# Kernel optimization log

Measured on AMD Instinct MI355X. Metric: run time of the kernel, lower is better.

The kernel has to match this reference:

```python
import jax, jax.numpy as jnp
import numpy as np

V, E, HD, T = 50000, 300, 512, 9   # vocab, embed_dim, hidden_dim, tagset
H = HD // 2                         # per-direction LSTM hidden
B, S = 64, 512


def _uniform(key, shape, k):
    return jax.random.uniform(key, shape, jnp.float32, -k, k)


def setup_inputs() -> dict:
    key = jax.random.key(0)
    ks = jax.random.split(key, 16)
    klstm = 1.0 / np.sqrt(H)
    kout = 1.0 / np.sqrt(HD)
    embed = jax.random.normal(ks[0], (V, E), jnp.float32) * 0.1
    embed = embed.at[0].set(0.0)  # padding_idx=0
    inp = {
        'sentence': jax.random.randint(ks[1], (B, S), 1, V),
        'tags': jax.random.randint(ks[2], (B, S), 0, T),
        'embed': embed,
        'wih_f': _uniform(ks[3], (4 * H, E), klstm),
        'whh_f': _uniform(ks[4], (4 * H, H), klstm),
        'bih_f': _uniform(ks[5], (4 * H,), klstm),
        'bhh_f': _uniform(ks[6], (4 * H,), klstm),
        'wih_b': _uniform(ks[7], (4 * H, E), klstm),
        'whh_b': _uniform(ks[8], (4 * H, H), klstm),
        'bih_b': _uniform(ks[9], (4 * H,), klstm),
        'bhh_b': _uniform(ks[10], (4 * H,), klstm),
        'w_out': _uniform(ks[11], (T, HD), kout),
        'b_out': _uniform(ks[12], (T,), kout),
        'start_trans': _uniform(ks[13], (T,), 0.1),
        'end_trans': _uniform(ks[14], (T,), 0.1),
        'trans': _uniform(ks[15], (T, T), 0.1),
    }
    # contiguous left-aligned mask with random lengths (mask[:,0]==1 as torchcrf requires)
    lengths = jax.random.randint(jax.random.fold_in(key, 99), (B,), S // 2, S + 1)
    inp['mask'] = (jnp.arange(S)[None, :] < lengths[:, None]).astype(jnp.int32)
    return inp


def _lstm(x, wih, whh, bih, bhh):
    # x: [S,B,E] -> hidden states [S,B,H]; gate order i,f,g,o (PyTorch)
    b = x.shape[1]
    def step(carry, xt):
        h, c = carry
        g = xt @ wih.T + h @ whh.T + (bih + bhh)
        i, f, gg, o = jnp.split(g, 4, axis=-1)
        c = jax.nn.sigmoid(f) * c + jax.nn.sigmoid(i) * jnp.tanh(gg)
        h = jax.nn.sigmoid(o) * jnp.tanh(c)
        return (h, c), h
    init = (jnp.zeros((b, H), x.dtype), jnp.zeros((b, H), x.dtype))
    _, hs = jax.lax.scan(step, init, x)
    return hs


def _forward(sentence, tags, mask, embed, wih_f, whh_f, bih_f, bhh_f,
             wih_b, whh_b, bih_b, bhh_b, w_out, b_out,
             start_trans, end_trans, trans):
    # dropout in eval mode -> identity
    x = embed[sentence].transpose(1, 0, 2)                # [S,B,E]
    hf = _lstm(x, wih_f, whh_f, bih_f, bhh_f)             # [S,B,H]
    hb = _lstm(x[::-1], wih_b, whh_b, bih_b, bhh_b)[::-1]  # [S,B,H]
    hcat = jnp.concatenate([hf, hb], axis=-1)             # [S,B,HD]
    emis = hcat @ w_out.T + b_out                         # [S,B,T]

    mask_t = mask.T.astype(bool)                          # [S,B]
    tags_t = tags.T                                       # [S,B]
    bar = jnp.arange(tags.shape[0])

    # --- numerator: gold path score ---
    score = start_trans[tags_t[0]] + emis[0, bar, tags_t[0]]
    tr_sc = trans[tags_t[:-1], tags_t[1:]]                # [S-1,B]
    em_sc = jnp.take_along_axis(emis[1:], tags_t[1:][..., None], axis=-1)[..., 0]
    score = score + ((tr_sc + em_sc) * mask_t[1:].astype(emis.dtype)).sum(0)
    lengths = mask.astype(jnp.int32).sum(1)
    last_tags = tags[bar, lengths - 1]
    score = score + end_trans[last_tags]

    # --- denominator: forward algorithm (logsumexp DP over tags) ---
    alpha0 = start_trans[None, :] + emis[0]               # [B,T]
    def step(alpha, inp):
        em_i, m_i = inp
        nxt = jax.nn.logsumexp(alpha[:, :, None] + trans[None] + em_i[:, None, :], axis=1)
        return jnp.where(m_i[:, None], nxt, alpha), None
    alpha, _ = jax.lax.scan(step, alpha0, (emis[1:], mask_t[1:]))
    logZ = jax.nn.logsumexp(alpha + end_trans[None, :], axis=1)

    llh = score - logZ
    return -llh.mean()  # torchcrf reduction='mean', negated


def reference(sentence, tags, mask, embed, wih_f, whh_f, bih_f, bhh_f,
              wih_b, whh_b, bih_b, bhh_b, w_out, b_out,
              start_trans, end_trans, trans):
    return _forward(sentence, tags, mask, embed, wih_f, whh_f, bih_f, bhh_f,
                    wih_b, whh_b, bih_b, bhh_b, w_out, b_out,
                    start_trans, end_trans, trans)
```

## Files before the change

kernel.cpp:

```cpp
#include <hip/hip_runtime.h>
#include <hip/hip_bf16.h>
#include <hip/hip_fp8.h>
#include <stdint.h>

#define EDIM 300
#define KP   320
#define HDIM 256
#define G4H  1024
#define NB   2048
#define TAGS 9
#define BATCH 64
#define SEQ  512
#define MROWS (SEQ*BATCH)

typedef _Float16 f16;
typedef _Float16 half2_t __attribute__((ext_vector_type(2)));
typedef _Float16 half8_t __attribute__((ext_vector_type(8)));
typedef float    floatx4 __attribute__((ext_vector_type(4)));
typedef uint32_t u32x2   __attribute__((ext_vector_type(2)));

__device__ __forceinline__ float fast_sigmoid(float x) {
    return __builtin_amdgcn_rcpf(1.f + __expf(-x));
}
__device__ __forceinline__ float fast_tanh(float x) {
    return 1.f - 2.f*__builtin_amdgcn_rcpf(__expf(2.f*x) + 1.f);
}
__device__ __forceinline__ uint8_t to_e4m3(float x) {
    __hip_fp8_e4m3 q(x);
    return __builtin_bit_cast(uint8_t, q);
}

__global__ void k_pack_wih(const float* __restrict__ wih_f, const float* __restrict__ wih_b,
                           const float* __restrict__ bih_f, const float* __restrict__ bhh_f,
                           const float* __restrict__ bih_b, const float* __restrict__ bhh_b,
                           f16* __restrict__ wpack, float* __restrict__ bias2) {
    int n = blockIdx.x;
    const float* src = (n < G4H) ? (wih_f + (long)n*EDIM) : (wih_b + (long)(n-G4H)*EDIM);
    for (int k = threadIdx.x; k < KP; k += 64)
        wpack[(long)n*KP + k] = (k < EDIM) ? (f16)src[k] : (f16)0.f;
    if (threadIdx.x == 0)
        bias2[n] = (n < G4H) ? (bih_f[n] + bhh_f[n]) : (bih_b[n-G4H] + bhh_b[n-G4H]);
}

__global__ void k_pack_whh8(const float* __restrict__ whh_f, const float* __restrict__ whh_b,
                            uint8_t* __restrict__ whhp8) {
    int idx = blockIdx.x*256 + threadIdx.x;
    int lane = idx & 63;
    int kf = (idx >> 6) & 7;
    int fr = (idx >> 9) & 15;
    int w  = (idx >> 13) & 3;
    int dir = idx >> 15;
    const float* whh = dir ? whh_b : whh_f;
    int grow = (fr >> 2)*256 + w*64 + (fr & 3)*16 + (lane & 15);
    int k0 = kf*32 + (lane >> 4)*8;
    const float* src = whh + (long)grow*HDIM + k0;
    uint8_t tmp[8];
    #pragma unroll
    for (int j = 0; j < 8; ++j) tmp[j] = to_e4m3(src[j] * 16.f);
    *(uint2*)(whhp8 + (size_t)idx*8) = *(uint2*)tmp;
}

__global__ void k_gather(const int* __restrict__ sentence, const float* __restrict__ embed,
                         f16* __restrict__ xg) {
    int m = blockIdx.x;
    int t = m >> 6, b = m & 63;
    int tok = sentence[b*SEQ + t];
    const float* row = embed + (long)tok*EDIM;
    for (int e = threadIdx.x; e < KP; e += 64)
        xg[(long)m*KP + e] = (e < EDIM) ? (f16)row[e] : (f16)0.f;
}

__launch_bounds__(256)
__global__ void k_gemm_xproj(const f16* __restrict__ xg, const f16* __restrict__ wpack,
                             const float* __restrict__ bias2, f16* __restrict__ xp5) {
    __shared__ __align__(16) f16 As[128*40];
    __shared__ __align__(16) f16 Bs[128*40];
    int tid = threadIdx.x;
    int bm = blockIdx.x, bn = blockIdx.y;
    int wid = tid >> 6, lane = tid & 63;
    int waveM = wid & 1, waveN = wid >> 1;
    int quad = lane >> 4, mlo = lane & 15;
    int c0 = tid,        r0 = c0 >> 2, o0 = (c0 & 3)*8;
    int c1 = tid + 256,  r1 = c1 >> 2, o1 = (c1 & 3)*8;
    const f16* ag = xg    + (long)(bm*128)*KP;
    const f16* bg = wpack + (long)(bn*128)*KP;
    uint4 pa0 = *(const uint4*)(&ag[(long)r0*KP + o0]);
    uint4 pa1 = *(const uint4*)(&ag[(long)r1*KP + o1]);
    uint4 pb0 = *(const uint4*)(&bg[(long)r0*KP + o0]);
    uint4 pb1 = *(const uint4*)(&bg[(long)r1*KP + o1]);
    floatx4 acc[4][4] = {};
    for (int k0 = 0; k0 < KP; k0 += 32) {
        *(uint4*)(&As[r0*40 + o0]) = pa0;
        *(uint4*)(&As[r1*40 + o1]) = pa1;
        *(uint4*)(&Bs[r0*40 + o0]) = pb0;
        *(uint4*)(&Bs[r1*40 + o1]) = pb1;
        __syncthreads();
        if (k0 + 32 < KP) {
            pa0 = *(const uint4*)(&ag[(long)r0*KP + k0+32 + o0]);
            pa1 = *(const uint4*)(&ag[(long)r1*KP + k0+32 + o1]);
            pb0 = *(const uint4*)(&bg[(long)r0*KP + k0+32 + o0]);
            pb1 = *(const uint4*)(&bg[(long)r1*KP + k0+32 + o1]);
        }
        half8_t af[4], bf[4];
        #pragma unroll
        for (int i = 0; i < 4; ++i)
            af[i] = *(const half8_t*)(&As[(waveM*64 + i*16 + mlo)*40 + quad*8]);
        #pragma unroll
        for (int j = 0; j < 4; ++j)
            bf[j] = *(const half8_t*)(&Bs[(waveN*64 + j*16 + mlo)*40 + quad*8]);
        #pragma unroll
        for (int i = 0; i < 4; ++i)
            #pragma unroll
            for (int j = 0; j < 4; ++j)
                acc[i][j] = __builtin_amdgcn_mfma_f32_16x16x32_f16(af[i], bf[j], acc[i][j], 0, 0, 0);
        __syncthreads();
    }
    #pragma unroll
    for (int i = 0; i < 4; ++i)
        #pragma unroll
        for (int j = 0; j < 4; ++j) {
            int col = bn*128 + waveN*64 + j*16 + mlo;
            float bv = bias2[col];
            int dir = col >> 10, grow = col & 1023;
            int gate = grow >> 8, u = grow & 255;
            int rowp = u*4 + gate;
            #pragma unroll
            for (int r = 0; r < 4; ++r) {
                int row = bm*128 + waveM*64 + i*16 + quad*4 + r;
                int t = row >> 6, bb = row & 63;
                int s = dir ? (SEQ-1-t) : t;
                xp5[((size_t)(dir*64 + bb)*512 + s)*1024 + rowp] = (f16)(acc[i][j][r] + bv);
            }
        }
}

__launch_bounds__(256, 1)
__global__ void k_recur(const f16* __restrict__ xp5, const uint8_t* __restrict__ whhp8,
                        f16* __restrict__ hcat) {
    __shared__ __align__(16) float gbuf[4][16][16];
    __shared__ __align__(8) uint8_t hbuf[2][256];
    int dir = blockIdx.x & 1, b = blockIdx.x >> 1;
    int tid = threadIdx.x, w = tid >> 6, lane = tid & 63;
    int q = lane >> 4;
    int v = lane;

    const uint8_t* wbase = whhp8 + (size_t)(dir*4 + w)*65536;
    u32x2 wa[128];
    #pragma unroll
    for (int g = 0; g < 128; ++g)
        wa[g] = *(const u32x2*)(wbase + ((size_t)g*64 + lane)*8);

    if (tid < 64) ((uint32_t*)&hbuf[0][0])[tid] = 0u;

    const f16* xs = xp5 + ((size_t)(dir*64 + b)*512)*1024 + (w*64 + v)*4;
    uint2 xw = *(const uint2*)xs;

    floatx4 zc = {0.f, 0.f, 0.f, 0.f};
    float cc = 0.f;
    __syncthreads();

    for (int s = 0; s < SEQ; ++s) {
        int t = dir ? (SEQ-1-s) : s;
        int sp = (s+1 < SEQ) ? s+1 : s;
        uint2 xn = *(const uint2*)(xs + (size_t)sp*1024);
        floatx4 acc[16];
        const uint8_t* hp = &hbuf[s & 1][0];
        #pragma unroll
        for (int kf = 0; kf < 8; ++kf) {
            u32x2 bf2 = *(const u32x2*)(hp + kf*32 + q*8);
            #pragma unroll
            for (int fr = 0; fr < 16; ++fr) {
                const int g = fr*8 + kf;
                if (kf == 0)
                    asm("v_mfma_f32_16x16x32_fp8_fp8 %0, %1, %2, %3"
                        : "=&v"(acc[fr]) : "a"(wa[g]), "v"(bf2), "v"(zc));
                else
                    asm("v_mfma_f32_16x16x32_fp8_fp8 %0, %1, %2, %0"
                        : "+v"(acc[fr]) : "a"(wa[g]), "v"(bf2));
            }
        }
        if ((lane & 15) == 0) {
            #pragma unroll
            for (int fr = 0; fr < 16; ++fr)
                *(floatx4*)&gbuf[w][fr][q*4] = acc[fr];
        }
        {
            const float is = 1.f/256.f;
            int sub = v >> 4, rr = v & 15;
            half2_t xif = __builtin_bit_cast(half2_t, xw.x);
            half2_t xgo = __builtin_bit_cast(half2_t, xw.y);
            float pi = __builtin_fmaf(gbuf[w][0  + sub][rr], is, (float)xif[0]);
            float pf = __builtin_fmaf(gbuf[w][4  + sub][rr], is, (float)xif[1]);
            float pg = __builtin_fmaf(gbuf[w][8  + sub][rr], is, (float)xgo[0]);
            float po = __builtin_fmaf(gbuf[w][12 + sub][rr], is, (float)xgo[1]);
            float si = fast_sigmoid(pi), sf = fast_sigmoid(pf);
            float tg = fast_tanh(pg),   so = fast_sigmoid(po);
            cc = __builtin_fmaf(sf, cc, si*tg);
            float hh = so * fast_tanh(cc);
            hbuf[(s+1) & 1][w*64 + v] = to_e4m3(hh * 16.f);
            hcat[((size_t)t*64 + b)*512 + dir*HDIM + w*64 + v] = (f16)hh;
        }
        xw = xn;
        asm volatile("s_waitcnt lgkmcnt(0)" ::: "memory");
        __builtin_amdgcn_s_barrier();
        asm volatile("" ::: "memory");
    }
}

__launch_bounds__(256)
__global__ void k_emis(const f16* __restrict__ hcat, const float* __restrict__ w_out,
                       const float* __restrict__ b_out, float* __restrict__ emis) {
    int r = blockIdx.x*4 + (threadIdx.x >> 6);
    int lane = threadIdx.x & 63;
    float hv[8];
    #pragma unroll
    for (int i = 0; i < 8; ++i) hv[i] = (float)hcat[(long)r*512 + lane + i*64];
    for (int tag = 0; tag < TAGS; ++tag) {
        float acc = 0.f;
        #pragma unroll
        for (int i = 0; i < 8; ++i) acc += hv[i]*w_out[tag*512 + lane + i*64];
        for (int off = 32; off; off >>= 1) acc += __shfl_xor(acc, off);
        if (lane == 0) emis[(long)r*TAGS + tag] = acc + b_out[tag];
    }
}

__launch_bounds__(256)
__global__ void k_crf(const float* __restrict__ emis, const int* __restrict__ tags,
                      const int* __restrict__ mask, const float* __restrict__ start_trans,
                      const float* __restrict__ end_trans, const float* __restrict__ trans,
                      float* __restrict__ out) {
    int b = blockIdx.x*4 + (threadIdx.x >> 6);
    int lane = threadIdx.x & 63;
    int len = 0;
    #pragma unroll
    for (int i = 0; i < 8; ++i) len += mask[b*SEQ + lane + i*64];
    for (int off = 32; off; off >>= 1) len += __shfl_xor(len, off);
    float sc = 0.f;
    for (int i = 0; i < 8; ++i) {
        int t = 1 + lane + i*64;
        if (t < SEQ && mask[b*SEQ + t]) {
            int tp = tags[b*SEQ + t - 1], tc = tags[b*SEQ + t];
            sc += trans[tp*TAGS + tc] + emis[(long)(t*64 + b)*TAGS + tc];
        }
    }
    for (int off = 32; off; off >>= 1) sc += __shfl_xor(sc, off);
    int tag0 = tags[b*SEQ];
    sc += start_trans[tag0] + emis[(long)b*TAGS + tag0];
    sc += end_trans[tags[b*SEQ + len - 1]];
    bool act = lane < TAGS;
    int j = act ? lane : 0;
    float tcol[TAGS];
    #pragma unroll
    for (int i = 0; i < TAGS; ++i) tcol[i] = trans[i*TAGS + j];
    float alpha = act ? (start_trans[j] + emis[(long)b*TAGS + j]) : -1e30f;
    for (int t = 1; t < SEQ; ++t) {
        int mt = mask[b*SEQ + t];
        float em = emis[(long)(t*64 + b)*TAGS + j];
        float v[TAGS], mx = -1e30f;
        #pragma unroll
        for (int i = 0; i < TAGS; ++i) { v[i] = __shfl(alpha, i) + tcol[i]; mx = fmaxf(mx, v[i]); }
        float ss = 0.f;
        #pragma unroll
        for (int i = 0; i < TAGS; ++i) ss += __expf(v[i] - mx);
        float nxt = mx + __logf(ss) + em;
        if (mt && act) alpha = nxt;
    }
    float fv = act ? (alpha + end_trans[j]) : -1e30f;
    float mx = fv;
    for (int off = 32; off; off >>= 1) mx = fmaxf(mx, __shfl_xor(mx, off));
    float ss = act ? __expf(fv - mx) : 0.f;
    for (int off = 32; off; off >>= 1) ss += __shfl_xor(ss, off);
    float logZ = mx + __logf(ss);
    if (lane == 0) atomicAdd(out, (logZ - sc) * (1.0f/BATCH));
}

extern "C" void kernel_launch(void* const* d_in, const int* in_sizes, int n_in,
                              void* d_out, int out_size, void* d_ws, size_t ws_size,
                              hipStream_t stream) {
    const int*   sentence    = (const int*)  d_in[0];
    const int*   tags        = (const int*)  d_in[1];
    const float* embed       = (const float*)d_in[2];
    const float* wih_f       = (const float*)d_in[3];
    const float* whh_f       = (const float*)d_in[4];
    const float* bih_f       = (const float*)d_in[5];
    const float* bhh_f       = (const float*)d_in[6];
    const float* wih_b       = (const float*)d_in[7];
    const float* whh_b       = (const float*)d_in[8];
    const float* bih_b       = (const float*)d_in[9];
    const float* bhh_b       = (const float*)d_in[10];
    const float* w_out       = (const float*)d_in[11];
    const float* b_out       = (const float*)d_in[12];
    const float* start_trans = (const float*)d_in[13];
    const float* end_trans   = (const float*)d_in[14];
    const float* trans       = (const float*)d_in[15];
    const int*   mask        = (const int*)  d_in[16];

    char* ws = (char*)d_ws;
    f16*     xg     = (f16*)ws;     ws += (size_t)MROWS*KP*2;
    f16*     wpack  = (f16*)ws;     ws += (size_t)NB*KP*2;
    float*   bias2  = (float*)ws;   ws += (size_t)NB*4;
    uint8_t* whhp8  = (uint8_t*)ws; ws += (size_t)1024*512;
    f16*     xp5    = (f16*)ws;     ws += (size_t)MROWS*NB*2;
    f16*     hcat   = (f16*)ws;     ws += (size_t)MROWS*512*2;
    float*   emis   = (float*)ws;   ws += (size_t)MROWS*TAGS*4;

    hipLaunchKernelGGL(k_pack_wih, dim3(NB), dim3(64), 0, stream,
                       wih_f, wih_b, bih_f, bhh_f, bih_b, bhh_b, wpack, bias2);
    hipLaunchKernelGGL(k_pack_whh8, dim3(256), dim3(256), 0, stream, whh_f, whh_b, whhp8);
    hipLaunchKernelGGL(k_gather, dim3(MROWS), dim3(64), 0, stream, sentence, embed, xg);
    hipLaunchKernelGGL(k_gemm_xproj, dim3(256,16), dim3(256), 0, stream, xg, wpack, bias2, xp5);
    hipLaunchKernelGGL(k_recur, dim3(128), dim3(256), 0, stream, xp5, whhp8, hcat);
    hipLaunchKernelGGL(k_emis, dim3(MROWS/4), dim3(256), 0, stream, hcat, w_out, b_out, emis);
    hipMemsetAsync(d_out, 0, sizeof(float), stream);
    hipLaunchKernelGGL(k_crf, dim3(BATCH/4), dim3(256), 0, stream,
                       emis, tags, mask, start_trans, end_trans, trans, (float*)d_out);
}
```

Baseline: 1.237 ms.

## Read LSTM gate accumulators from registers instead of LDS scratch buffer

The recurrent kernel used to write the MFMA gate accumulators to a shared-memory buffer and read them back per hidden unit. Now each lane picks its four gate values straight from its own accumulator registers through selects, with the hidden-unit index remapped to match the MFMA output layout. The input-projection GEMM now stores gates in natural gate-major order, so each lane loads four scalar f16 values per step instead of one packed 8-byte load. This removes LDS traffic and latency from the serial per-step critical path, at the cost of extra select instructions and less coalesced x-projection loads.

```diff
diff --git a/kernel.cpp b/kernel.cpp
--- a/kernel.cpp
+++ b/kernel.cpp
@@ -72,7 +72,7 @@
 
 __launch_bounds__(256)
 __global__ void k_gemm_xproj(const f16* __restrict__ xg, const f16* __restrict__ wpack,
-                             const float* __restrict__ bias2, f16* __restrict__ xp5) {
+                             const float* __restrict__ bias2, f16* __restrict__ xp6) {
     __shared__ __align__(16) f16 As[128*40];
     __shared__ __align__(16) f16 Bs[128*40];
     int tid = threadIdx.x;
@@ -122,27 +122,28 @@
             int col = bn*128 + waveN*64 + j*16 + mlo;
             float bv = bias2[col];
             int dir = col >> 10, grow = col & 1023;
-            int gate = grow >> 8, u = grow & 255;
-            int rowp = u*4 + gate;
             #pragma unroll
             for (int r = 0; r < 4; ++r) {
                 int row = bm*128 + waveM*64 + i*16 + quad*4 + r;
                 int t = row >> 6, bb = row & 63;
                 int s = dir ? (SEQ-1-t) : t;
-                xp5[((size_t)(dir*64 + bb)*512 + s)*1024 + rowp] = (f16)(acc[i][j][r] + bv);
+                xp6[((size_t)(dir*64 + bb)*512 + s)*1024 + grow] = (f16)(acc[i][j][r] + bv);
             }
         }
 }
 
 __launch_bounds__(256, 1)
-__global__ void k_recur(const f16* __restrict__ xp5, const uint8_t* __restrict__ whhp8,
+__global__ void k_recur(const f16* __restrict__ xp6, const uint8_t* __restrict__ whhp8,
                         f16* __restrict__ hcat) {
-    __shared__ __align__(16) float gbuf[4][16][16];
     __shared__ __align__(8) uint8_t hbuf[2][256];
     int dir = blockIdx.x & 1, b = blockIdx.x >> 1;
     int tid = threadIdx.x, w = tid >> 6, lane = tid & 63;
     int q = lane >> 4;
-    int v = lane;
+    int cc4 = lane & 15;
+    int sub = cc4 >> 2, rsel = cc4 & 3;
+    int u = sub*16 + q*4 + rsel;
+    bool rlo = (rsel & 1) != 0, rhi = (rsel >> 1) != 0;
+    bool slo = (sub  & 1) != 0, shi = (sub  >> 1) != 0;
 
     const uint8_t* wbase = whhp8 + (size_t)(dir*4 + w)*65536;
     u32x2 wa[128];
@@ -152,8 +153,10 @@
 
     if (tid < 64) ((uint32_t*)&hbuf[0][0])[tid] = 0u;
 
-    const f16* xs = xp5 + ((size_t)(dir*64 + b)*512)*1024 + (w*64 + v)*4;
-    uint2 xw = *(const uint2*)xs;
+    const f16* xs = xp6 + ((size_t)(dir*64 + b)*512)*1024 + w*64 + u;
+    float xv[4];
+    #pragma unroll
+    for (int g = 0; g < 4; ++g) xv[g] = (float)xs[g*256];
 
     floatx4 zc = {0.f, 0.f, 0.f, 0.f};
     float cc = 0.f;
@@ -162,7 +165,9 @@
     for (int s = 0; s < SEQ; ++s) {
         int t = dir ? (SEQ-1-s) : s;
         int sp = (s+1 < SEQ) ? s+1 : s;
-        uint2 xn = *(const uint2*)(xs + (size_t)sp*1024);
+        float xn[4];
+        #pragma unroll
+        for (int g = 0; g < 4; ++g) xn[g] = (float)xs[(size_t)sp*1024 + g*256];
         floatx4 acc[16];
         const uint8_t* hp = &hbuf[s & 1][0];
         #pragma unroll
@@ -179,28 +184,34 @@
                         : "+v"(acc[fr]) : "a"(wa[g]), "v"(bf2));
             }
         }
-        if ((lane & 15) == 0) {
-            #pragma unroll
-            for (int fr = 0; fr < 16; ++fr)
-                *(floatx4*)&gbuf[w][fr][q*4] = acc[fr];
+        float gv[4];
+        #pragma unroll
+        for (int g = 0; g < 4; ++g) {
+            float s0, s1, s2, s3;
+            {
+                const int f0 = g*4 + 0, f1 = g*4 + 1, f2 = g*4 + 2, f3 = g*4 + 3;
+                s0 = rlo ? (rhi ? acc[f0][3] : acc[f0][1]) : (rhi ? acc[f0][2] : acc[f0][0]);
+                s1 = rlo ? (rhi ? acc[f1][3] : acc[f1][1]) : (rhi ? acc[f1][2] : acc[f1][0]);
+                s2 = rlo ? (rhi ? acc[f2][3] : acc[f2][1]) : (rhi ? acc[f2][2] : acc[f2][0]);
+                s3 = rlo ? (rhi ? acc[f3][3] : acc[f3][1]) : (rhi ? acc[f3][2] : acc[f3][0]);
+            }
+            gv[g] = slo ? (shi ? s3 : s1) : (shi ? s2 : s0);
         }
         {
             const float is = 1.f/256.f;
-            int sub = v >> 4, rr = v & 15;
-            half2_t xif = __builtin_bit_cast(half2_t, xw.x);
-            half2_t xgo = __builtin_bit_cast(half2_t, xw.y);
-            float pi = __builtin_fmaf(gbuf[w][0  + sub][rr], is, (float)xif[0]);
-            float pf = __builtin_fmaf(gbuf[w][4  + sub][rr], is, (float)xif[1]);
-            float pg = __builtin_fmaf(gbuf[w][8  + sub][rr], is, (float)xgo[0]);
-            float po = __builtin_fmaf(gbuf[w][12 + sub][rr], is, (float)xgo[1]);
+            float pi = __builtin_fmaf(gv[0], is, xv[0]);
+            float pf = __builtin_fmaf(gv[1], is, xv[1]);
+            float pg = __builtin_fmaf(gv[2], is, xv[2]);
+            float po = __builtin_fmaf(gv[3], is, xv[3]);
             float si = fast_sigmoid(pi), sf = fast_sigmoid(pf);
             float tg = fast_tanh(pg),   so = fast_sigmoid(po);
             cc = __builtin_fmaf(sf, cc, si*tg);
             float hh = so * fast_tanh(cc);
-            hbuf[(s+1) & 1][w*64 + v] = to_e4m3(hh * 16.f);
-            hcat[((size_t)t*64 + b)*512 + dir*HDIM + w*64 + v] = (f16)hh;
-        }
-        xw = xn;
+            hbuf[(s+1) & 1][w*64 + u] = to_e4m3(hh * 16.f);
+            hcat[((size_t)t*64 + b)*512 + dir*HDIM + w*64 + u] = (f16)hh;
+        }
+        #pragma unroll
+        for (int g = 0; g < 4; ++g) xv[g] = xn[g];
         asm volatile("s_waitcnt lgkmcnt(0)" ::: "memory");
         __builtin_amdgcn_s_barrier();
         asm volatile("" ::: "memory");
@@ -300,7 +311,7 @@
     f16*     wpack  = (f16*)ws;     ws += (size_t)NB*KP*2;
     float*   bias2  = (float*)ws;   ws += (size_t)NB*4;
     uint8_t* whhp8  = (uint8_t*)ws; ws += (size_t)1024*512;
-    f16*     xp5    = (f16*)ws;     ws += (size_t)MROWS*NB*2;
+    f16*     xp6    = (f16*)ws;     ws += (size_t)MROWS*NB*2;
     f16*     hcat   = (f16*)ws;     ws += (size_t)MROWS*512*2;
     float*   emis   = (float*)ws;   ws += (size_t)MROWS*TAGS*4;
 
@@ -308,8 +319,8 @@
                        wih_f, wih_b, bih_f, bhh_f, bih_b, bhh_b, wpack, bias2);
     hipLaunchKernelGGL(k_pack_whh8, dim3(256), dim3(256), 0, stream, whh_f, whh_b, whhp8);
     hipLaunchKernelGGL(k_gather, dim3(MROWS), dim3(64), 0, stream, sentence, embed, xg);
-    hipLaunchKernelGGL(k_gemm_xproj, dim3(256,16), dim3(256), 0, stream, xg, wpack, bias2, xp5);
-    hipLaunchKernelGGL(k_recur, dim3(128), dim3(256), 0, stream, xp5, whhp8, hcat);
+    hipLaunchKernelGGL(k_gemm_xproj, dim3(256,16), dim3(256), 0, stream, xg, wpack, bias2, xp6);
+    hipLaunchKernelGGL(k_recur, dim3(128), dim3(256), 0, stream, xp6, whhp8, hcat);
     hipLaunchKernelGGL(k_emis, dim3(MROWS/4), dim3(256), 0, stream, hcat, w_out, b_out, emis);
     hipMemsetAsync(d_out, 0, sizeof(float), stream);
     hipLaunchKernelGGL(k_crf, dim3(BATCH/4), dim3(256), 0, stream,
```

Measured after the change: 1.028 ms. 16.9% less time.
